# Kernel tuning notes

Measured on AMD Instinct MI355X. Metric: run time of the kernel, lower is better.

## Reference

```python
import jax, jax.numpy as jnp
import numpy as np

N_NODES = 50000
N_EDGES = 800000
IN_CH = 128
HEADS = 4
OUT_CH = 32
NEG_SLOPE = 0.2


def setup_inputs() -> dict:
    key = jax.random.key(0)
    ks = jax.random.split(key, 7)
    x = jax.random.normal(ks[0], (N_NODES, IN_CH), dtype=jnp.float32)
    src = jax.random.randint(ks[1], (N_EDGES,), 0, N_NODES, dtype=jnp.int32)
    dst = jax.random.randint(ks[2], (N_EDGES,), 0, N_NODES, dtype=jnp.int32)
    W = jax.random.normal(ks[3], (IN_CH, HEADS * OUT_CH), dtype=jnp.float32) * (1.0 / np.sqrt(IN_CH))
    attn_l = jax.random.normal(ks[4], (HEADS, OUT_CH), dtype=jnp.float32) * 0.1
    attn_r = jax.random.normal(ks[5], (HEADS, OUT_CH), dtype=jnp.float32) * 0.1
    bias = jnp.zeros((HEADS * OUT_CH,), dtype=jnp.float32)
    return {"x": x, "src": src, "dst": dst, "W": W, "attn_l": attn_l, "attn_r": attn_r, "bias": bias}


def reference(x, src, dst, W, attn_l, attn_r, bias):
    n = x.shape[0]
    # Linear projection -> per-head features [N, H, D]
    feat = (x @ W).reshape(n, HEADS, OUT_CH)
    # Node-level attention terms [N, H]
    el = jnp.einsum('nhd,hd->nh', feat, attn_l)
    er = jnp.einsum('nhd,hd->nh', feat, attn_r)
    # Edge attention logits [E, H]
    e = jax.nn.leaky_relu(el[src] + er[dst], negative_slope=NEG_SLOPE)
    # Segment softmax over incoming edges of each dst node
    m = jax.ops.segment_max(e, dst, num_segments=n)          # [N, H]
    m = jnp.where(jnp.isfinite(m), m, 0.0)
    ex = jnp.exp(e - m[dst])                                  # [E, H]
    s = jax.ops.segment_sum(ex, dst, num_segments=n)          # [N, H]
    alpha = ex / s[dst]                                       # [E, H]
    # Weighted message aggregation: scatter-add to dst [N, H, D]
    msg = feat[src] * alpha[:, :, None]
    out = jax.ops.segment_sum(msg, dst, num_segments=n)
    out = out + bias.reshape(HEADS, OUT_CH)
    # agg='mean' over heads -> [N, D]
    return out.mean(axis=1)
```

## Files before the change

kernel.cpp:

```cpp
#include <hip/hip_runtime.h>

#define IN_CH 128
#define NEG_SLOPE 0.2f
#define MAXDEG 64

#define NPB 256
#define NBUCK 196
#define ECHUNK 4096
#define EBLK 196
#define CAP 56

typedef short bf16x8 __attribute__((ext_vector_type(8)));
typedef float floatx4 __attribute__((ext_vector_type(4)));

static __device__ __forceinline__ unsigned short f2bf(float f) {
    union { float f; unsigned int u; } a; a.f = f;
    unsigned int u = a.u;
    u += 0x7fffu + ((u >> 16) & 1u);
    return (unsigned short)(u >> 16);
}

__global__ void k_prep(const float* __restrict__ W, unsigned short* __restrict__ Wtb) {
    int i = blockIdx.x * 256 + threadIdx.x;
    if (i < 128 * 128) {
        int n = i >> 7, k = i & 127;
        Wtb[i] = f2bf(W[(size_t)k * 128 + n]);
    }
}

__global__ __launch_bounds__(256) void k_fused(const float* __restrict__ x,
                                               const unsigned short* __restrict__ Wtb,
                                               const float* __restrict__ attn_l,
                                               const float* __restrict__ attn_r,
                                               unsigned short* __restrict__ featb,
                                               float* __restrict__ el,
                                               float* __restrict__ er, int N,
                                               const int* __restrict__ src,
                                               const int* __restrict__ dst,
                                               unsigned int* __restrict__ gseg,
                                               unsigned char* __restrict__ cnt8, int E,
                                               int GB) {
    __shared__ __align__(16) unsigned short Al[16 * 136];
    __shared__ float elpart[2][8][16];
    __shared__ int lcnt[NBUCK];
    int b = blockIdx.x;
    bool is_edge;
    int part;
    if (b < 2 * EBLK) { is_edge = (b & 1); part = b >> 1; }
    else              { is_edge = false;   part = b - EBLK; }
    if (is_edge) {
        for (int i = threadIdx.x; i < NBUCK; i += 256) lcnt[i] = 0;
        __syncthreads();
        int base = part * ECHUNK;
#pragma unroll
        for (int k = 0; k < ECHUNK / 256; ++k) {
            int e = base + k * 256 + threadIdx.x;
            if (e < E) {
                int dn = dst[e];
                int sv = src[e];
                int bkt = dn >> 8;
                int r = atomicAdd(&lcnt[bkt], 1);
                if (r < CAP)
                    gseg[((size_t)bkt * EBLK + part) * CAP + r] =
                        ((unsigned int)dn << 16) | (unsigned int)sv;
            }
        }
        __syncthreads();
        for (int i = threadIdx.x; i < NBUCK; i += 256) {
            int c = lcnt[i]; if (c > CAP) c = CAP;
            cnt8[(size_t)part * 256 + i] = (unsigned char)c;
        }
        return;
    }
    int m0 = part * 16;
    const float4* xt = (const float4*)(x + (size_t)m0 * 128);
#pragma unroll
    for (int i = 0; i < 2; ++i) {
        int f4i = threadIdx.x + 256 * i;
        float4 u = xt[f4i];
        int f = f4i * 4;
        int row = f >> 7, col = f & 127;
        ushort4 pk;
        pk.x = f2bf(u.x); pk.y = f2bf(u.y); pk.z = f2bf(u.z); pk.w = f2bf(u.w);
        *(ushort4*)(Al + row * 136 + col) = pk;
    }
    __syncthreads();
    int wave = threadIdx.x >> 6;
    int lane = threadIdx.x & 63;
    int l15 = lane & 15;
    int quad = lane >> 4;
    int n0 = wave * 16;
    int n1 = wave * 16 + 64;
    const unsigned short* ap = Al + l15 * 136 + quad * 8;
    const unsigned short* bp0 = Wtb + (size_t)(n0 + l15) * 128 + quad * 8;
    const unsigned short* bp1 = Wtb + (size_t)(n1 + l15) * 128 + quad * 8;
    floatx4 acc0 = {0.f, 0.f, 0.f, 0.f};
    floatx4 acc1 = {0.f, 0.f, 0.f, 0.f};
#pragma unroll
    for (int kk = 0; kk < 4; ++kk) {
        bf16x8 a  = *(const bf16x8*)(ap + kk * 32);
        bf16x8 b0 = *(const bf16x8*)(bp0 + kk * 32);
        bf16x8 b1 = *(const bf16x8*)(bp1 + kk * 32);
        acc0 = __builtin_amdgcn_mfma_f32_16x16x32_bf16(a, b0, acc0, 0, 0, 0);
        acc1 = __builtin_amdgcn_mfma_f32_16x16x32_bf16(a, b1, acc1, 0, 0, 0);
    }
    float al0 = attn_l[n0 + l15], al1 = attn_l[n1 + l15];
    float ar0 = attn_r[n0 + l15], ar1 = attn_r[n1 + l15];
    float pl0[4], pl1[4], pr0[4], pr1[4];
#pragma unroll
    for (int r = 0; r < 4; ++r) {
        pl0[r] = acc0[r] * al0; pl1[r] = acc1[r] * al1;
        pr0[r] = acc0[r] * ar0; pr1[r] = acc1[r] * ar1;
#pragma unroll
        for (int m = 1; m <= 8; m <<= 1) {
            pl0[r] += __shfl_xor(pl0[r], m);
            pl1[r] += __shfl_xor(pl1[r], m);
            pr0[r] += __shfl_xor(pr0[r], m);
            pr1[r] += __shfl_xor(pr1[r], m);
        }
    }
    if (l15 == 0) {
#pragma unroll
        for (int r = 0; r < 4; ++r) {
            int row = quad * 4 + r;
            elpart[0][wave][row]     = pl0[r];
            elpart[0][wave + 4][row] = pl1[r];
            elpart[1][wave][row]     = pr0[r];
            elpart[1][wave + 4][row] = pr1[r];
        }
    }
#pragma unroll
    for (int r = 0; r < 4; ++r) {
        size_t row = (size_t)(m0 + quad * 4 + r) * 128;
        featb[row + n0 + l15] = f2bf(acc0[r]);
        featb[row + n1 + l15] = f2bf(acc1[r]);
    }
    __syncthreads();
    if (threadIdx.x < 128) {
        int lr = threadIdx.x >> 6;
        int t = threadIdx.x & 63;
        int row = t & 15, h = t >> 4;
        float v = elpart[lr][2 * h][row] + elpart[lr][2 * h + 1][row];
        float* dp = lr ? er : el;
        dp[(size_t)(m0 + row) * 4 + h] = v;
    }
}

__global__ __launch_bounds__(256) void k_bucket(const unsigned int* __restrict__ gseg,
                                                const unsigned char* __restrict__ cnt8,
                                                unsigned short* __restrict__ esrc_pad,
                                                int* __restrict__ cnt, int N) {
    __shared__ unsigned short adj[NPB * MAXDEG];
    __shared__ int ndeg[NPB];
    __shared__ unsigned char c8[EBLK];
    int bkt = blockIdx.x;
    for (int i = threadIdx.x; i < NPB; i += 256) ndeg[i] = 0;
    for (int i = threadIdx.x; i < EBLK; i += 256) c8[i] = cnt8[(size_t)i * 256 + bkt];
    __syncthreads();
    const unsigned int* seg = gseg + (size_t)bkt * EBLK * CAP;
    const int total = EBLK * CAP;
    for (int s = threadIdx.x; s < total; s += 256) {
        int blk = s / CAP;
        int slot = s - blk * CAP;
        if (slot < (int)c8[blk]) {
            unsigned int ed = seg[s];
            int ln = (int)(ed >> 16) & (NPB - 1);
            int r = atomicAdd(&ndeg[ln], 1);
            if (r < MAXDEG) adj[ln * MAXDEG + r] = (unsigned short)(ed & 0xffffu);
        }
    }
    __syncthreads();
    int n0 = bkt * NPB;
    int nvalid = N - n0; if (nvalid > NPB) nvalid = NPB;
    if (nvalid <= 0) return;
    int words = nvalid * (MAXDEG / 8);
    const uint4* asrc = (const uint4*)adj;
    uint4* adst = (uint4*)(esrc_pad + (size_t)n0 * MAXDEG);
    for (int i = threadIdx.x; i < words; i += 256) adst[i] = asrc[i];
    for (int i = threadIdx.x; i < nvalid; i += 256) cnt[n0 + i] = ndeg[i];
}

__global__ __launch_bounds__(256) void k_node(const int* __restrict__ cnt,
                                              const unsigned short* __restrict__ esrc_pad,
                                              const float* __restrict__ el,
                                              const float* __restrict__ er,
                                              const unsigned short* __restrict__ featb,
                                              const float* __restrict__ bias,
                                              float* __restrict__ out, int N) {
    int n = blockIdx.x * 4 + (threadIdx.x >> 6);
    if (n >= N) return;
    int lane = threadIdx.x & 63;
    int g = lane >> 4;
    int r = lane & 15;
    int h = r >> 2;
    int deg = cnt[n];
    if (deg > MAXDEG) deg = MAXDEG;
    const unsigned short* ep = esrc_pad + (size_t)n * MAXDEG;
    float erh = er[(size_t)n * 4 + h];
    float s = 0.f;
    float a0 = 0.f, a1 = 0.f, a2 = 0.f, a3 = 0.f;
    float a4 = 0.f, a5 = 0.f, a6 = 0.f, a7 = 0.f;
    int j = g;
    int sn_c = (j < deg) ? (int)ep[j] : 0;
    float el_c = el[(size_t)sn_c * 4 + h];
    uint4 q_c = *(const uint4*)(featb + (size_t)sn_c * 128 + r * 8);
#pragma unroll 2
    for (; j < deg; j += 4) {
        int jn = j + 4;
        int sn_n = (jn < deg) ? (int)ep[jn] : 0;
        float el_n = el[(size_t)sn_n * 4 + h];
        uint4 q_n = *(const uint4*)(featb + (size_t)sn_n * 128 + r * 8);
        float t = el_c + erh;
        float e = __expf(t > 0.f ? t : NEG_SLOPE * t);
        s += e;
        a0 += e * __uint_as_float(q_c.x << 16);
        a1 += e * __uint_as_float(q_c.x & 0xffff0000u);
        a2 += e * __uint_as_float(q_c.y << 16);
        a3 += e * __uint_as_float(q_c.y & 0xffff0000u);
        a4 += e * __uint_as_float(q_c.z << 16);
        a5 += e * __uint_as_float(q_c.z & 0xffff0000u);
        a6 += e * __uint_as_float(q_c.w << 16);
        a7 += e * __uint_as_float(q_c.w & 0xffff0000u);
        sn_c = sn_n; el_c = el_n; q_c = q_n;
    }
    s  += __shfl_xor(s, 16);  s  += __shfl_xor(s, 32);
    a0 += __shfl_xor(a0, 16); a0 += __shfl_xor(a0, 32);
    a1 += __shfl_xor(a1, 16); a1 += __shfl_xor(a1, 32);
    a2 += __shfl_xor(a2, 16); a2 += __shfl_xor(a2, 32);
    a3 += __shfl_xor(a3, 16); a3 += __shfl_xor(a3, 32);
    a4 += __shfl_xor(a4, 16); a4 += __shfl_xor(a4, 32);
    a5 += __shfl_xor(a5, 16); a5 += __shfl_xor(a5, 32);
    a6 += __shfl_xor(a6, 16); a6 += __shfl_xor(a6, 32);
    a7 += __shfl_xor(a7, 16); a7 += __shfl_xor(a7, 32);
    float inv = (deg > 0) ? 0.25f / s : 0.f;
    a0 *= inv; a1 *= inv; a2 *= inv; a3 *= inv;
    a4 *= inv; a5 *= inv; a6 *= inv; a7 *= inv;
    a0 += __shfl_xor(a0, 4); a0 += __shfl_xor(a0, 8);
    a1 += __shfl_xor(a1, 4); a1 += __shfl_xor(a1, 8);
    a2 += __shfl_xor(a2, 4); a2 += __shfl_xor(a2, 8);
    a3 += __shfl_xor(a3, 4); a3 += __shfl_xor(a3, 8);
    a4 += __shfl_xor(a4, 4); a4 += __shfl_xor(a4, 8);
    a5 += __shfl_xor(a5, 4); a5 += __shfl_xor(a5, 8);
    a6 += __shfl_xor(a6, 4); a6 += __shfl_xor(a6, 8);
    a7 += __shfl_xor(a7, 4); a7 += __shfl_xor(a7, 8);
    if (lane < 4) {
        int dd = lane * 8;
        float4 o0, o1;
        o0.x = a0 + 0.25f * (bias[dd + 0] + bias[32 + dd + 0] + bias[64 + dd + 0] + bias[96 + dd + 0]);
        o0.y = a1 + 0.25f * (bias[dd + 1] + bias[32 + dd + 1] + bias[64 + dd + 1] + bias[96 + dd + 1]);
        o0.z = a2 + 0.25f * (bias[dd + 2] + bias[32 + dd + 2] + bias[64 + dd + 2] + bias[96 + dd + 2]);
        o0.w = a3 + 0.25f * (bias[dd + 3] + bias[32 + dd + 3] + bias[64 + dd + 3] + bias[96 + dd + 3]);
        o1.x = a4 + 0.25f * (bias[dd + 4] + bias[32 + dd + 4] + bias[64 + dd + 4] + bias[96 + dd + 4]);
        o1.y = a5 + 0.25f * (bias[dd + 5] + bias[32 + dd + 5] + bias[64 + dd + 5] + bias[96 + dd + 5]);
        o1.z = a6 + 0.25f * (bias[dd + 6] + bias[32 + dd + 6] + bias[64 + dd + 6] + bias[96 + dd + 6]);
        o1.w = a7 + 0.25f * (bias[dd + 7] + bias[32 + dd + 7] + bias[64 + dd + 7] + bias[96 + dd + 7]);
        *(float4*)(out + (size_t)n * 32 + dd) = o0;
        *(float4*)(out + (size_t)n * 32 + dd + 4) = o1;
    }
}

extern "C" void kernel_launch(void* const* d_in, const int* in_sizes, int n_in,
                              void* d_out, int out_size, void* d_ws, size_t ws_size,
                              hipStream_t stream) {
    const float* x      = (const float*)d_in[0];
    const int*   src    = (const int*)d_in[1];
    const int*   dst    = (const int*)d_in[2];
    const float* W      = (const float*)d_in[3];
    const float* attn_l = (const float*)d_in[4];
    const float* attn_r = (const float*)d_in[5];
    const float* bias   = (const float*)d_in[6];
    float* out = (float*)d_out;

    int N = in_sizes[0] / IN_CH;
    int E = in_sizes[1];
    int GB = N / 16;

    char* w = (char*)d_ws;
    unsigned short* featb = (unsigned short*)w; w += (size_t)N * 128 * 2;
    unsigned short* Wtb   = (unsigned short*)w; w += 128 * 128 * 2;
    float* el       = (float*)w;  w += (size_t)N * 4 * 4;
    float* er       = (float*)w;  w += (size_t)N * 4 * 4;
    int*   cnt      = (int*)w;    w += (size_t)N * 4;
    unsigned short* esrc_pad = (unsigned short*)w; w += (size_t)N * MAXDEG * 2;
    unsigned int*   gseg = (unsigned int*)w; w += (size_t)NBUCK * EBLK * CAP * 4;
    unsigned char*  cnt8 = (unsigned char*)w; w += (size_t)EBLK * 256;

    k_prep<<<64, 256, 0, stream>>>(W, Wtb);
    k_fused<<<GB + EBLK, 256, 0, stream>>>(x, Wtb, attn_l, attn_r, featb, el, er, N,
                                           src, dst, gseg, cnt8, E, GB);
    k_bucket<<<NBUCK, 256, 0, stream>>>(gseg, cnt8, esrc_pad, cnt, N);
    k_node<<<(N + 3) / 4, 256, 0, stream>>>(cnt, esrc_pad, el, er, featb, bias, out, N);
}
```

Measured before the change: 161.1 us.

## Stage W in swizzled LDS and loop each GEMM block over four row tiles

Each projection block now handles 64 rows instead of 16. It first copies the full bf16 weight matrix into shared memory with an XOR swizzle, then loops over four 16-row tiles while prefetching the next x tile into registers. This cuts how often each block re-reads W from global memory or L2 and overlaps the x loads with the MFMA work. In exchange there are four times fewer GEMM blocks, and every block uses 32KB more shared memory, including the edge-bucketing blocks. That may reduce occupancy.

```diff
diff --git a/kernel.cpp b/kernel.cpp
--- a/kernel.cpp
+++ b/kernel.cpp
@@ -9,6 +9,8 @@
 #define ECHUNK 4096
 #define EBLK 196
 #define CAP 56
+
+#define GTILE 64
 
 typedef short bf16x8 __attribute__((ext_vector_type(8)));
 typedef float floatx4 __attribute__((ext_vector_type(4)));
@@ -38,8 +40,8 @@
                                                const int* __restrict__ src,
                                                const int* __restrict__ dst,
                                                unsigned int* __restrict__ gseg,
-                                               unsigned char* __restrict__ cnt8, int E,
-                                               int GB) {
+                                               unsigned char* __restrict__ cnt8, int E) {
+    __shared__ __align__(16) unsigned short Bl[128 * 128];
     __shared__ __align__(16) unsigned short Al[16 * 136];
     __shared__ float elpart[2][8][16];
     __shared__ int lcnt[NBUCK];
@@ -72,77 +74,124 @@
         }
         return;
     }
-    int m0 = part * 16;
-    const float4* xt = (const float4*)(x + (size_t)m0 * 128);
-#pragma unroll
-    for (int i = 0; i < 2; ++i) {
-        int f4i = threadIdx.x + 256 * i;
-        float4 u = xt[f4i];
-        int f = f4i * 4;
-        int row = f >> 7, col = f & 127;
-        ushort4 pk;
-        pk.x = f2bf(u.x); pk.y = f2bf(u.y); pk.z = f2bf(u.z); pk.w = f2bf(u.w);
-        *(ushort4*)(Al + row * 136 + col) = pk;
-    }
-    __syncthreads();
+
+    int base = part * GTILE;
+    int ntile = (N - base + 15) >> 4; if (ntile > 4) ntile = 4;
+
+    {
+        const uint4* wsrc = (const uint4*)Wtb;
+        char* blb = (char*)Bl;
+#pragma unroll
+        for (int ii = 0; ii < 8; ++ii) {
+            int idx16 = threadIdx.x + 256 * ii;
+            uint4 v = wsrc[idx16];
+            int n = idx16 >> 4;
+            int kb = (idx16 & 15) << 4;
+            *(uint4*)(blb + n * 256 + (kb ^ ((n & 7) << 4))) = v;
+        }
+    }
+
     int wave = threadIdx.x >> 6;
     int lane = threadIdx.x & 63;
     int l15 = lane & 15;
     int quad = lane >> 4;
     int n0 = wave * 16;
     int n1 = wave * 16 + 64;
-    const unsigned short* ap = Al + l15 * 136 + quad * 8;
-    const unsigned short* bp0 = Wtb + (size_t)(n0 + l15) * 128 + quad * 8;
-    const unsigned short* bp1 = Wtb + (size_t)(n1 + l15) * 128 + quad * 8;
-    floatx4 acc0 = {0.f, 0.f, 0.f, 0.f};
-    floatx4 acc1 = {0.f, 0.f, 0.f, 0.f};
-#pragma unroll
-    for (int kk = 0; kk < 4; ++kk) {
-        bf16x8 a  = *(const bf16x8*)(ap + kk * 32);
-        bf16x8 b0 = *(const bf16x8*)(bp0 + kk * 32);
-        bf16x8 b1 = *(const bf16x8*)(bp1 + kk * 32);
-        acc0 = __builtin_amdgcn_mfma_f32_16x16x32_bf16(a, b0, acc0, 0, 0, 0);
-        acc1 = __builtin_amdgcn_mfma_f32_16x16x32_bf16(a, b1, acc1, 0, 0, 0);
-    }
-    float al0 = attn_l[n0 + l15], al1 = attn_l[n1 + l15];
-    float ar0 = attn_r[n0 + l15], ar1 = attn_r[n1 + l15];
-    float pl0[4], pl1[4], pr0[4], pr1[4];
-#pragma unroll
-    for (int r = 0; r < 4; ++r) {
-        pl0[r] = acc0[r] * al0; pl1[r] = acc1[r] * al1;
-        pr0[r] = acc0[r] * ar0; pr1[r] = acc1[r] * ar1;
-#pragma unroll
-        for (int m = 1; m <= 8; m <<= 1) {
-            pl0[r] += __shfl_xor(pl0[r], m);
-            pl1[r] += __shfl_xor(pl1[r], m);
-            pr0[r] += __shfl_xor(pr0[r], m);
-            pr1[r] += __shfl_xor(pr1[r], m);
-        }
-    }
-    if (l15 == 0) {
+    int r0 = n0 + l15, r1 = n1 + l15;
+    const char* blb = (const char*)Bl;
+    int sw = (r0 & 7) << 4;
+    float al0 = attn_l[r0], al1 = attn_l[r1];
+    float ar0 = attn_r[r0], ar1 = attn_r[r1];
+
+    float4 xr[2];
+    {
+        const float4* xt = (const float4*)(x + (size_t)base * 128);
+#pragma unroll
+        for (int i = 0; i < 2; ++i) {
+            float4 u = xt[threadIdx.x + 256 * i];
+            int f = (threadIdx.x + 256 * i) * 4;
+            int row = f >> 7, col = f & 127;
+            ushort4 pk;
+            pk.x = f2bf(u.x); pk.y = f2bf(u.y); pk.z = f2bf(u.z); pk.w = f2bf(u.w);
+            *(ushort4*)(Al + row * 136 + col) = pk;
+        }
+        if (ntile > 1) {
+            const float4* xt1 = (const float4*)(x + (size_t)(base + 16) * 128);
+#pragma unroll
+            for (int i = 0; i < 2; ++i) xr[i] = xt1[threadIdx.x + 256 * i];
+        }
+    }
+    __syncthreads();
+
+    for (int t = 0; t < ntile; ++t) {
+        int m0 = base + t * 16;
+        const unsigned short* ap = Al + l15 * 136 + quad * 8;
+        floatx4 acc0 = {0.f, 0.f, 0.f, 0.f};
+        floatx4 acc1 = {0.f, 0.f, 0.f, 0.f};
+#pragma unroll
+        for (int kk = 0; kk < 4; ++kk) {
+            int kb = ((quad << 4) + (kk << 6));
+            bf16x8 a  = *(const bf16x8*)(ap + kk * 32);
+            bf16x8 b0 = *(const bf16x8*)(blb + r0 * 256 + (kb ^ sw));
+            bf16x8 b1 = *(const bf16x8*)(blb + r1 * 256 + (kb ^ sw));
+            acc0 = __builtin_amdgcn_mfma_f32_16x16x32_bf16(a, b0, acc0, 0, 0, 0);
+            acc1 = __builtin_amdgcn_mfma_f32_16x16x32_bf16(a, b1, acc1, 0, 0, 0);
+        }
+        float pl0[4], pl1[4], pr0[4], pr1[4];
 #pragma unroll
         for (int r = 0; r < 4; ++r) {
-            int row = quad * 4 + r;
-            elpart[0][wave][row]     = pl0[r];
-            elpart[0][wave + 4][row] = pl1[r];
-            elpart[1][wave][row]     = pr0[r];
-            elpart[1][wave + 4][row] = pr1[r];
-        }
-    }
-#pragma unroll
-    for (int r = 0; r < 4; ++r) {
-        size_t row = (size_t)(m0 + quad * 4 + r) * 128;
-        featb[row + n0 + l15] = f2bf(acc0[r]);
-        featb[row + n1 + l15] = f2bf(acc1[r]);
-    }
-    __syncthreads();
-    if (threadIdx.x < 128) {
-        int lr = threadIdx.x >> 6;
-        int t = threadIdx.x & 63;
-        int row = t & 15, h = t >> 4;
-        float v = elpart[lr][2 * h][row] + elpart[lr][2 * h + 1][row];
-        float* dp = lr ? er : el;
-        dp[(size_t)(m0 + row) * 4 + h] = v;
+            pl0[r] = acc0[r] * al0; pl1[r] = acc1[r] * al1;
+            pr0[r] = acc0[r] * ar0; pr1[r] = acc1[r] * ar1;
+#pragma unroll
+            for (int m = 1; m <= 8; m <<= 1) {
+                pl0[r] += __shfl_xor(pl0[r], m);
+                pl1[r] += __shfl_xor(pl1[r], m);
+                pr0[r] += __shfl_xor(pr0[r], m);
+                pr1[r] += __shfl_xor(pr1[r], m);
+            }
+        }
+        if (l15 == 0) {
+#pragma unroll
+            for (int r = 0; r < 4; ++r) {
+                int row = quad * 4 + r;
+                elpart[0][wave][row]     = pl0[r];
+                elpart[0][wave + 4][row] = pl1[r];
+                elpart[1][wave][row]     = pr0[r];
+                elpart[1][wave + 4][row] = pr1[r];
+            }
+        }
+#pragma unroll
+        for (int r = 0; r < 4; ++r) {
+            size_t row = (size_t)(m0 + quad * 4 + r) * 128;
+            featb[row + r0] = f2bf(acc0[r]);
+            featb[row + r1] = f2bf(acc1[r]);
+        }
+        __syncthreads();
+        if (threadIdx.x < 128) {
+            int lr = threadIdx.x >> 6;
+            int tt = threadIdx.x & 63;
+            int row = tt & 15, h = tt >> 4;
+            float v = elpart[lr][2 * h][row] + elpart[lr][2 * h + 1][row];
+            float* dp = lr ? er : el;
+            dp[(size_t)(m0 + row) * 4 + h] = v;
+        }
+        if (t + 1 < ntile) {
+#pragma unroll
+            for (int i = 0; i < 2; ++i) {
+                int f = (threadIdx.x + 256 * i) * 4;
+                int row = f >> 7, col = f & 127;
+                ushort4 pk;
+                pk.x = f2bf(xr[i].x); pk.y = f2bf(xr[i].y);
+                pk.z = f2bf(xr[i].z); pk.w = f2bf(xr[i].w);
+                *(ushort4*)(Al + row * 136 + col) = pk;
+            }
+            if (t + 2 < ntile) {
+                const float4* xt2 = (const float4*)(x + (size_t)(base + (t + 2) * 16) * 128);
+#pragma unroll
+                for (int i = 0; i < 2; ++i) xr[i] = xt2[threadIdx.x + 256 * i];
+            }
+        }
+        __syncthreads();
     }
 }
 
@@ -273,7 +322,7 @@
 
     int N = in_sizes[0] / IN_CH;
     int E = in_sizes[1];
-    int GB = N / 16;
+    int GB = (N + GTILE - 1) / GTILE;
 
     char* w = (char*)d_ws;
     unsigned short* featb = (unsigned short*)w; w += (size_t)N * 128 * 2;
@@ -287,7 +336,7 @@
 
     k_prep<<<64, 256, 0, stream>>>(W, Wtb);
     k_fused<<<GB + EBLK, 256, 0, stream>>>(x, Wtb, attn_l, attn_r, featb, el, er, N,
-                                           src, dst, gseg, cnt8, E, GB);
+                                           src, dst, gseg, cnt8, E);
     k_bucket<<<NBUCK, 256, 0, stream>>>(gseg, cnt8, esrc_pad, cnt, N);
     k_node<<<(N + 3) / 4, 256, 0, stream>>>(cnt, esrc_pad, el, er, featb, bias, out, N);
 }
```

Measured after the change: 155.4 us. -3.5%, faster.
